# Optimization experiments

Hardware: AMD Instinct MI355X
Metric: run time of the kernel (lower is better)

The kernel has to match this reference:

```python
import jax, jax.numpy as jnp
import numpy as np
import math

WIN = (24, 24)
NUM_HEADS = 16
RPB_DIM = 512
BS = 32
LOG2_8 = math.log2(8.0)  # 3.0


def _buffers():
    wh, ww = WIN
    # continuous log-scaled relative coordinate table: ((2wh-1)*(2ww-1), 2)
    rh = np.arange(-(wh - 1), wh, dtype=np.float32)
    rw = np.arange(-(ww - 1), ww, dtype=np.float32)
    table = np.stack(np.meshgrid(rh, rw, indexing='ij'), axis=-1)  # (2wh-1, 2ww-1, 2)
    table[..., 0] /= (wh - 1)
    table[..., 1] /= (ww - 1)
    table *= 8.0
    table = np.sign(table) * np.log2(np.abs(table) + 1.0) / LOG2_8
    coords_table = table.reshape(-1, 2).astype(np.float32)
    # relative position index: (N, N) with N = wh*ww
    ch = np.arange(wh)
    cw = np.arange(ww)
    coords = np.stack(np.meshgrid(ch, cw, indexing='ij'))  # (2, wh, ww)
    cf = coords.reshape(2, -1)                              # (2, N)
    rel = (cf[:, :, None] - cf[:, None, :]).transpose(1, 2, 0).copy()  # (N, N, 2)
    rel[:, :, 0] += wh - 1
    rel[:, :, 1] += ww - 1
    rel[:, :, 0] *= 2 * ww - 1
    rpi = rel.sum(-1).astype(np.int32)
    return coords_table, rpi


def setup_inputs() -> dict:
    key = jax.random.key(0)
    k1, k2, k3 = jax.random.split(key, 3)
    coords_table, rpi = _buffers()
    return {
        "glob_pos": jax.random.uniform(k1, (1, BS, 4), jnp.float32, 0.1, 1.0),
        "coords_table": jnp.asarray(coords_table),            # (T, 2)
        "rpi": jnp.asarray(rpi),                              # (N, N) int32
        "W1": jax.random.normal(k2, (2, RPB_DIM), jnp.float32) * 0.02,
        "b1": jnp.zeros((RPB_DIM,), jnp.float32),
        "W2": jax.random.normal(k3, (RPB_DIM, NUM_HEADS), jnp.float32) * 0.02,
        "num_prefix_tokens": 1,
    }


def reference(glob_pos, coords_table, rpi, W1, b1, W2, num_prefix_tokens):
    g = glob_pos[0]                       # squeeze(0) -> (bs, 4)
    pos_all = g[..., :2]                  # (bs, 2)
    pos = g[..., 2:]                      # (bs, 2)
    pos = (pos / pos_all) * 8.0
    pos = jnp.sign(pos) * jnp.log2(jnp.abs(pos) + 1.0) / LOG2_8
    pos = pos * 2.0 - 1.0
    # shifted coordinate table per sample: (bs, T, 2)
    table = coords_table[None, :, :] + pos[:, None, :]
    # tiny CPB MLP -> (bs, T, H)
    h = jax.nn.relu(jnp.einsum('btc,cd->btd', table, W1) + b1)
    bias = jnp.einsum('btd,dh->bth', h, W2)
    N = rpi.shape[0]
    bs = g.shape[0]
    H = W2.shape[1]
    P = num_prefix_tokens
    # gather per-pair bias: (bs, N, N, H)
    gathered = bias[:, rpi.reshape(-1)].reshape(bs, N, N, H)
    # zero-pad prefix rows/cols, then permute to (bs, H, N+P, N+P)
    result = jnp.zeros((bs, N + P, N + P, H), dtype=gathered.dtype)
    result = result.at[:, P:, P:].set(gathered)
    return jnp.transpose(result, (0, 3, 1, 2))
```

## Files before the change

### kernel.cpp

```cpp
#include <hip/hip_runtime.h>
#include <hip/hip_bf16.h>

#define TT    2209
#define NB    32
#define NH    16
#define ND    512
#define WH    24
#define NW    576
#define NP    577
#define PLANE (NP * NP)

__global__ __launch_bounds__(256) void cpb_mlp(
    const float* __restrict__ glob_pos,
    const float* __restrict__ coords_table,
    const float* __restrict__ W1,
    const float* __restrict__ b1,
    const float* __restrict__ W2,
    float* __restrict__ bias_t)
{
    __shared__ float sW13[ND][4];
    __shared__ float sW2[ND][NH];

    const int tid = threadIdx.x;
    for (int d = tid; d < ND; d += 256) {
        float4 v;
        v.x = W1[d];
        v.y = W1[ND + d];
        v.z = b1[d];
        v.w = 0.0f;
        *reinterpret_cast<float4*>(&sW13[d][0]) = v;
    }
    for (int i = tid; i < ND * NH / 4; i += 256) {
        reinterpret_cast<float4*>(&sW2[0][0])[i] =
            reinterpret_cast<const float4*>(W2)[i];
    }
    __syncthreads();

    const unsigned gid  = blockIdx.x * 256u + tid;
    const bool     live = gid < (unsigned)(NB * TT);
    const unsigned b    = live ? gid / TT : 0u;
    const unsigned t    = live ? gid - b * TT : 0u;

    const float g0 = glob_pos[b * 4 + 0];
    const float g1 = glob_pos[b * 4 + 1];
    const float g2 = glob_pos[b * 4 + 2];
    const float g3 = glob_pos[b * 4 + 3];
    float px = g2 / g0 * 8.0f;
    float py = g3 / g1 * 8.0f;
    px = copysignf(log2f(fabsf(px) + 1.0f) * (1.0f / 3.0f), px) * 2.0f - 1.0f;
    py = copysignf(log2f(fabsf(py) + 1.0f) * (1.0f / 3.0f), py) * 2.0f - 1.0f;

    const float tx = coords_table[t * 2 + 0] + px;
    const float ty = coords_table[t * 2 + 1] + py;

    float acc[NH];
#pragma unroll
    for (int h = 0; h < NH; ++h) acc[h] = 0.0f;

#pragma unroll 1
    for (int d0 = 0; d0 < ND; d0 += 4) {
        float hv[4];
#pragma unroll
        for (int k = 0; k < 4; ++k) {
            const float4 w = *reinterpret_cast<const float4*>(&sW13[d0 + k][0]);
            hv[k] = fmaxf(fmaf(tx, w.x, fmaf(ty, w.y, w.z)), 0.0f);
        }
#pragma unroll
        for (int k = 0; k < 4; ++k) {
            const float4 w0 = *reinterpret_cast<const float4*>(&sW2[d0 + k][0]);
            const float4 w1 = *reinterpret_cast<const float4*>(&sW2[d0 + k][4]);
            const float4 w2 = *reinterpret_cast<const float4*>(&sW2[d0 + k][8]);
            const float4 w3 = *reinterpret_cast<const float4*>(&sW2[d0 + k][12]);
            acc[0]  = fmaf(hv[k], w0.x, acc[0]);   acc[1]  = fmaf(hv[k], w0.y, acc[1]);
            acc[2]  = fmaf(hv[k], w0.z, acc[2]);   acc[3]  = fmaf(hv[k], w0.w, acc[3]);
            acc[4]  = fmaf(hv[k], w1.x, acc[4]);   acc[5]  = fmaf(hv[k], w1.y, acc[5]);
            acc[6]  = fmaf(hv[k], w1.z, acc[6]);   acc[7]  = fmaf(hv[k], w1.w, acc[7]);
            acc[8]  = fmaf(hv[k], w2.x, acc[8]);   acc[9]  = fmaf(hv[k], w2.y, acc[9]);
            acc[10] = fmaf(hv[k], w2.z, acc[10]);  acc[11] = fmaf(hv[k], w2.w, acc[11]);
            acc[12] = fmaf(hv[k], w3.x, acc[12]);  acc[13] = fmaf(hv[k], w3.y, acc[13]);
            acc[14] = fmaf(hv[k], w3.z, acc[14]);  acc[15] = fmaf(hv[k], w3.w, acc[15]);
        }
    }

    if (live) {
#pragma unroll
        for (int h = 0; h < NH; ++h) {
            bias_t[(b * NH + h) * TT + t] = acc[h];
        }
    }
}

#define ELEMS 8
#define CHUNK (256 * ELEMS)
#define CPB   ((PLANE + CHUNK - 1) / CHUNK)

__global__ __launch_bounds__(256) void cpb_scatter(
    const float* __restrict__ bias_t,
    float* __restrict__ out)
{
    __shared__ float sPlane[TT];

    const unsigned bx  = blockIdx.x;
    const unsigned p   = bx / CPB;
    const unsigned c   = bx - p * CPB;
    const unsigned tid = threadIdx.x;

    const float* __restrict__ plane = bias_t + (size_t)p * TT;
    for (unsigned idx = tid; idx < TT; idx += 256u) sPlane[idx] = plane[idx];
    __syncthreads();

    const unsigned cb = c * CHUNK;
    float* __restrict__ oplane = out + (size_t)p * PLANE;

#pragma unroll
    for (int k = 0; k < ELEMS; ++k) {
        const unsigned off = cb + tid + 256u * (unsigned)k;
        if (off < (unsigned)PLANE) {
            const unsigned i = off / NP;
            const unsigned j = off - i * NP;
            float v = 0.0f;
            if (i != 0u && j != 0u) {
                const unsigned q  = i - 1u;
                const unsigned kk = j - 1u;
                const unsigned qh = q / WH,  qw = q - qh * WH;
                const unsigned kh = kk / WH, kw = kk - kh * WH;
                v = sPlane[(qh - kh + (WH - 1u)) * (2u * WH - 1u)
                           + (qw - kw + (WH - 1u))];
            }
            oplane[off] = v;
        }
    }
}

extern "C" void kernel_launch(void* const* d_in, const int* in_sizes, int n_in,
                              void* d_out, int out_size, void* d_ws, size_t ws_size,
                              hipStream_t stream)
{
    const float* glob_pos     = (const float*)d_in[0];
    const float* coords_table = (const float*)d_in[1];
    const float* W1           = (const float*)d_in[3];
    const float* b1           = (const float*)d_in[4];
    const float* W2           = (const float*)d_in[5];

    float* out    = (float*)d_out;
    float* bias_t = (float*)d_ws;

    const int n1 = NB * TT;
    const int blocks1 = (n1 + 255) / 256;
    cpb_mlp<<<blocks1, 256, 0, stream>>>(glob_pos, coords_table, W1, b1, W2, bias_t);

    const unsigned blocks2 = (unsigned)NB * NH * CPB;
    cpb_scatter<<<blocks2, 256, 0, stream>>>(bias_t, out);
}
```

Before: 886.4 us.

## Flatten scatter over all planes with float4 nontemporal stores and larger per-block work

The scatter kernel now treats the whole output as one flat array and gives each block a large contiguous span (41 float4 per thread). Each thread builds a float4 from up to two staged bias planes, since a span can cross a plane boundary, and writes it with a nontemporal vector store. The aim is wider, streaming writes and fewer blocks, so store throughput on this write-bound output improves. In exchange there are two shared-memory plane loads per block and more index arithmetic per element, and the float4 stores rely on the 16-byte alignment the flat offset gives.

```diff
diff --git a/kernel.cpp b/kernel.cpp
--- a/kernel.cpp
+++ b/kernel.cpp
@@ -9,6 +9,8 @@
 #define NW    576
 #define NP    577
 #define PLANE (NP * NP)
+
+typedef float vfloat4 __attribute__((ext_vector_type(4)));
 
 __global__ __launch_bounds__(256) void cpb_mlp(
     const float* __restrict__ glob_pos,
@@ -90,44 +92,62 @@
     }
 }
 
-#define ELEMS 8
-#define CHUNK (256 * ELEMS)
-#define CPB   ((PLANE + CHUNK - 1) / CHUNK)
+#define VPT   41u
+#define GPB   (256u * VPT)
+#define EPB   (GPB * 4u)
 
 __global__ __launch_bounds__(256) void cpb_scatter(
     const float* __restrict__ bias_t,
     float* __restrict__ out)
 {
-    __shared__ float sPlane[TT];
+    constexpr unsigned TOTAL = (unsigned)NB * NH * PLANE;
 
-    const unsigned bx  = blockIdx.x;
-    const unsigned p   = bx / CPB;
-    const unsigned c   = bx - p * CPB;
-    const unsigned tid = threadIdx.x;
+    const unsigned bx    = blockIdx.x;
+    const unsigned tid   = threadIdx.x;
+    const unsigned ebase = bx * EPB;
+    if (ebase >= TOTAL) return;
 
-    const float* __restrict__ plane = bias_t + (size_t)p * TT;
-    for (unsigned idx = tid; idx < TT; idx += 256u) sPlane[idx] = plane[idx];
+    __shared__ float sA[TT];
+    __shared__ float sB[TT];
+
+    const unsigned eend = min(ebase + EPB, TOTAL);
+    const unsigned pA   = ebase / PLANE;
+    const unsigned pB   = (eend - 1u) / PLANE;
+    const float* __restrict__ plA = bias_t + (size_t)pA * TT;
+    const float* __restrict__ plB = bias_t + (size_t)pB * TT;
+    for (unsigned x = tid; x < (unsigned)TT; x += 256u) {
+        sA[x] = plA[x];
+        sB[x] = plB[x];
+    }
     __syncthreads();
 
-    const unsigned cb = c * CHUNK;
-    float* __restrict__ oplane = out + (size_t)p * PLANE;
-
+#pragma unroll 2
+    for (unsigned k = 0; k < VPT; ++k) {
+        const unsigned off = ebase + (k * 256u + tid) * 4u;
+        if (off < TOTAL) {
+            const unsigned p0   = off / PLANE;
+            const unsigned rem0 = off - p0 * PLANE;
+            vfloat4 o;
 #pragma unroll
-    for (int k = 0; k < ELEMS; ++k) {
-        const unsigned off = cb + tid + 256u * (unsigned)k;
-        if (off < (unsigned)PLANE) {
-            const unsigned i = off / NP;
-            const unsigned j = off - i * NP;
-            float v = 0.0f;
-            if (i != 0u && j != 0u) {
-                const unsigned q  = i - 1u;
-                const unsigned kk = j - 1u;
-                const unsigned qh = q / WH,  qw = q - qh * WH;
-                const unsigned kh = kk / WH, kw = kk - kh * WH;
-                v = sPlane[(qh - kh + (WH - 1u)) * (2u * WH - 1u)
-                           + (qw - kw + (WH - 1u))];
+            for (int d = 0; d < 4; ++d) {
+                unsigned pp = p0;
+                unsigned ee = rem0 + (unsigned)d;
+                if (ee >= (unsigned)PLANE) { ee -= (unsigned)PLANE; ++pp; }
+                const float* __restrict__ s = (pp == pA) ? sA : sB;
+                const unsigned i = ee / NP;
+                const unsigned j = ee - i * NP;
+                float v = 0.0f;
+                if (i != 0u && j != 0u) {
+                    const unsigned q  = i - 1u;
+                    const unsigned kk = j - 1u;
+                    const unsigned qh = q / WH,  qw = q - qh * WH;
+                    const unsigned kh = kk / WH, kw = kk - kh * WH;
+                    v = s[(qh - kh + (WH - 1u)) * (2u * WH - 1u)
+                          + (qw - kw + (WH - 1u))];
+                }
+                o[d] = v;
             }
-            oplane[off] = v;
+            __builtin_nontemporal_store(o, reinterpret_cast<vfloat4*>(out + off));
         }
     }
 }
@@ -149,6 +169,7 @@
     const int blocks1 = (n1 + 255) / 256;
     cpb_mlp<<<blocks1, 256, 0, stream>>>(glob_pos, coords_table, W1, b1, W2, bias_t);
 
-    const unsigned blocks2 = (unsigned)NB * NH * CPB;
+    constexpr unsigned TOTAL  = (unsigned)NB * NH * PLANE;
+    const unsigned blocks2 = (TOTAL + EPB - 1u) / EPB;
     cpb_scatter<<<blocks2, 256, 0, stream>>>(bias_t, out);
 }
```

Result: faster. 730.5 us (-17.6%).

## Vectorize scatter stores with float4, fewer larger blocks, cheaper index math

Applied to the files above, without the earlier changes.

Rewrites the scatter kernel so each 512-thread block covers an eighth of a plane and writes aligned float4 groups, with scalar head and tail handling for misalignment. Index computation replaces divisions by 24 with a multiply-shift and folds the 2-D relative index into a single linear offset. The aim is fewer, wider global store instructions and less integer work on a store-bound kernel. In exchange each block loads the full 2209-entry table for fewer outputs, and the alignment and tail bookkeeping adds complexity.

```diff
diff --git a/kernel.cpp b/kernel.cpp
--- a/kernel.cpp
+++ b/kernel.cpp
@@ -90,45 +90,69 @@
     }
 }
 
-#define ELEMS 8
-#define CHUNK (256 * ELEMS)
-#define CPB   ((PLANE + CHUNK - 1) / CHUNK)
+#define CHUNK_ELEMS 41620u
 
-__global__ __launch_bounds__(256) void cpb_scatter(
+__device__ __forceinline__ float cpb_val(const float* __restrict__ sP,
+                                         unsigned i, unsigned j)
+{
+    const unsigned qi = i ? i - 1u : 0u;
+    const unsigned tj = j ? j - 1u : 0u;
+    const unsigned ai = qi + 23u * ((qi * 2731u) >> 16);
+    const unsigned aj = tj + 23u * ((tj * 2731u) >> 16);
+    const float v = sP[1104u + ai - aj];
+    return (i != 0u && j != 0u) ? v : 0.0f;
+}
+
+__global__ __launch_bounds__(512) void cpb_scatter(
     const float* __restrict__ bias_t,
     float* __restrict__ out)
 {
-    __shared__ float sPlane[TT];
-
     const unsigned bx  = blockIdx.x;
-    const unsigned p   = bx / CPB;
-    const unsigned c   = bx - p * CPB;
+    const unsigned p   = bx >> 3;
+    const unsigned c   = bx & 7u;
     const unsigned tid = threadIdx.x;
 
-    const float* __restrict__ plane = bias_t + (size_t)p * TT;
-    for (unsigned idx = tid; idx < TT; idx += 256u) sPlane[idx] = plane[idx];
+    __shared__ float sP[TT];
+    const float* __restrict__ pl = bias_t + (size_t)p * TT;
+    for (unsigned x = tid; x < (unsigned)TT; x += 512u) sP[x] = pl[x];
     __syncthreads();
 
-    const unsigned cb = c * CHUNK;
-    float* __restrict__ oplane = out + (size_t)p * PLANE;
+    const unsigned lbeg = c * CHUNK_ELEMS;
+    const unsigned lend = min(lbeg + CHUNK_ELEMS, (unsigned)PLANE);
+    const size_t   gofs = (size_t)p * PLANE;
 
+    const unsigned galign = (unsigned)((gofs + lbeg) & 3u);
+    const unsigned h0     = (4u - galign) & 3u;
+    const unsigned bbeg   = lbeg + h0;
+    const unsigned bspan  = (lend > bbeg) ? ((lend - bbeg) & ~3u) : 0u;
+    const unsigned bend   = bbeg + bspan;
+    const unsigned tcount = lend - bend;
+
+    if (tid < h0) {
+        const unsigned e = lbeg + tid;
+        const unsigned i = e / NP;
+        const unsigned j = e - i * NP;
+        out[gofs + e] = cpb_val(sP, i, j);
+    }
+    if (tid >= 64u && tid < 64u + tcount) {
+        const unsigned e = bend + (tid - 64u);
+        const unsigned i = e / NP;
+        const unsigned j = e - i * NP;
+        out[gofs + e] = cpb_val(sP, i, j);
+    }
+
+    const unsigned ngroups = bspan >> 2;
+    for (unsigned g = tid; g < ngroups; g += 512u) {
+        const unsigned e0 = bbeg + (g << 2);
+        unsigned i = e0 / NP;
+        unsigned j = e0 - i * NP;
+        float4 o;
 #pragma unroll
-    for (int k = 0; k < ELEMS; ++k) {
-        const unsigned off = cb + tid + 256u * (unsigned)k;
-        if (off < (unsigned)PLANE) {
-            const unsigned i = off / NP;
-            const unsigned j = off - i * NP;
-            float v = 0.0f;
-            if (i != 0u && j != 0u) {
-                const unsigned q  = i - 1u;
-                const unsigned kk = j - 1u;
-                const unsigned qh = q / WH,  qw = q - qh * WH;
-                const unsigned kh = kk / WH, kw = kk - kh * WH;
-                v = sPlane[(qh - kh + (WH - 1u)) * (2u * WH - 1u)
-                           + (qw - kw + (WH - 1u))];
-            }
-            oplane[off] = v;
+        for (int d = 0; d < 4; ++d) {
+            (&o.x)[d] = cpb_val(sP, i, j);
+            if (++j == (unsigned)NP) { j = 0u; ++i; }
         }
+        *reinterpret_cast<float4*>(out + gofs + e0) = o;
     }
 }
 
@@ -149,6 +173,6 @@
     const int blocks1 = (n1 + 255) / 256;
     cpb_mlp<<<blocks1, 256, 0, stream>>>(glob_pos, coords_table, W1, b1, W2, bias_t);
 
-    const unsigned blocks2 = (unsigned)NB * NH * CPB;
-    cpb_scatter<<<blocks2, 256, 0, stream>>>(bias_t, out);
+    const unsigned blocks2 = (unsigned)NB * NH * 8u;
+    cpb_scatter<<<blocks2, 512, 0, stream>>>(bias_t, out);
 }
```

Result: faster. 825.8 us (-6.8%).
